# Kernel tuning notes

Measured on AMD Instinct MI355X. Metric: run time of the kernel, lower is better.

The kernel has to match this reference:

```python
import jax, jax.numpy as jnp
import numpy as np

D = 512          # model_dim
H = 4 * D        # hidden_mult * model_dim
E = 8            # n_experts
TEMP = 1.0       # temperature
EPS = 1e-5       # torch LayerNorm eps


def setup_inputs() -> dict:
    key = jax.random.key(0)
    ks = jax.random.split(key, 6)
    x = jax.random.normal(ks[0], (4, 4096, D), dtype=jnp.float32)
    # gate: LayerNorm(D) + Linear(D, E)
    gate_gamma = jnp.ones((D,), jnp.float32)
    gate_beta = jnp.zeros((D,), jnp.float32)
    gate_W = jax.random.normal(ks[1], (D, E), jnp.float32) * 0.02
    gate_b = jnp.zeros((E,), jnp.float32)
    # experts stacked along leading E axis: Linear(D,H) -> LeakyReLU -> Linear(H,D)
    W1 = jax.random.normal(ks[2], (E, D, H), jnp.float32) * 0.02
    b1 = jnp.zeros((E, H), jnp.float32)
    W2 = jax.random.normal(ks[3], (E, H, D), jnp.float32) * 0.02
    b2 = jnp.zeros((E, D), jnp.float32)
    return {"x": x, "gate_gamma": gate_gamma, "gate_beta": gate_beta,
            "gate_W": gate_W, "gate_b": gate_b,
            "W1": W1, "b1": b1, "W2": W2, "b2": b2}


def reference(x, gate_gamma, gate_beta, gate_W, gate_b, W1, b1, W2, b2):
    # gate: LayerNorm then Linear, temperature-scaled softmax
    mu = jnp.mean(x, axis=-1, keepdims=True)
    var = jnp.var(x, axis=-1, keepdims=True)  # biased, as in torch LayerNorm
    xn = (x - mu) * jax.lax.rsqrt(var + EPS) * gate_gamma + gate_beta
    logits = (xn @ gate_W + gate_b) / TEMP          # [B,N,E]
    w = jax.nn.softmax(logits, axis=-1)             # [B,N,E]
    # run every expert on all tokens (faithful to soft routing)
    h = jnp.einsum('bnd,edh->benh', x, W1) + b1[None, :, None, :]  # [B,E,N,H]
    h = jax.nn.leaky_relu(h, negative_slope=0.01)
    y = jnp.einsum('benh,ehd->bend', h, W2) + b2[None, :, None, :]  # [B,E,N,D]
    # gate-weighted combine over experts
    out = jnp.einsum('bend,bne->bnd', y, w)
    return out
```

## Files before the change

kernel.cpp:

```cpp
#include <hip/hip_runtime.h>
#include <stdint.h>

#define TD 512
#define TH 2048
#define TE 8
#define TT 16384

typedef __bf16 bf16x8 __attribute__((ext_vector_type(8)));
typedef float  f32x4  __attribute__((ext_vector_type(4)));

__device__ __forceinline__ void async16(const void* src, void* lds) {
    __builtin_amdgcn_global_load_lds((const __attribute__((address_space(1))) uint32_t*)src,
                                     (__attribute__((address_space(3))) uint32_t*)lds,
                                     16, 0, 0);
}

__global__ __launch_bounds__(256) void gate_kernel(
    const float* __restrict__ x, const float* __restrict__ gamma,
    const float* __restrict__ beta, const float* __restrict__ gW,
    const float* __restrict__ gb, const float* __restrict__ b2,
    float* __restrict__ gate_w, __bf16* __restrict__ xb,
    float* __restrict__ outp)
{
    const int t    = blockIdx.x * 4 + (threadIdx.x >> 6);
    const int lane = threadIdx.x & 63;

    const float* xr = x + (size_t)t * TD + lane * 8;
    float4 v0 = *(const float4*)xr;
    float4 v1 = *(const float4*)(xr + 4);
    float xv[8] = {v0.x, v0.y, v0.z, v0.w, v1.x, v1.y, v1.z, v1.w};

    float s = 0.f, sq = 0.f;
    #pragma unroll
    for (int j = 0; j < 8; ++j) { s += xv[j]; sq += xv[j] * xv[j]; }
    #pragma unroll
    for (int off = 32; off > 0; off >>= 1) {
        s  += __shfl_xor(s, off);
        sq += __shfl_xor(sq, off);
    }
    const float mean = s * (1.f / TD);
    const float var  = sq * (1.f / TD) - mean * mean;
    const float rs   = rsqrtf(var + 1e-5f);

    bf16x8 xc;
    #pragma unroll
    for (int j = 0; j < 8; ++j) xc[j] = (__bf16)xv[j];
    *(bf16x8*)&xb[(size_t)t * TD + lane * 8] = xc;

    float p[TE] = {};
    #pragma unroll
    for (int j = 0; j < 8; ++j) {
        const int d = lane * 8 + j;
        const float xn = (xv[j] - mean) * rs * gamma[d] + beta[d];
        const float* wr = gW + (size_t)d * TE;
        #pragma unroll
        for (int e = 0; e < TE; ++e) p[e] += xn * wr[e];
    }
    #pragma unroll
    for (int off = 32; off > 0; off >>= 1) {
        #pragma unroll
        for (int e = 0; e < TE; ++e) p[e] += __shfl_xor(p[e], off);
    }

    float m = -3.4e38f;
    #pragma unroll
    for (int e = 0; e < TE; ++e) { p[e] += gb[e]; m = fmaxf(m, p[e]); }
    float sum = 0.f;
    #pragma unroll
    for (int e = 0; e < TE; ++e) { p[e] = expf(p[e] - m); sum += p[e]; }
    const float inv = 1.f / sum;
    if (lane == 0) {
        #pragma unroll
        for (int e = 0; e < TE; ++e) gate_w[(size_t)t * TE + e] = p[e] * inv;
    }

    float ob[8] = {};
    #pragma unroll
    for (int e = 0; e < TE; ++e) {
        const float we = p[e] * inv;
        const float* b2r = b2 + (size_t)e * TD + lane * 8;
        #pragma unroll
        for (int j = 0; j < 8; ++j) ob[j] += we * b2r[j];
    }
    float4 o0 = {ob[0], ob[1], ob[2], ob[3]};
    float4 o1 = {ob[4], ob[5], ob[6], ob[7]};
    *(float4*)&outp[(size_t)t * TD + lane * 8]     = o0;
    *(float4*)&outp[(size_t)t * TD + lane * 8 + 4] = o1;
}

__global__ __launch_bounds__(256) void tcast(
    const float* __restrict__ src, __bf16* __restrict__ dst, int R, int C)
{
    __shared__ __bf16 tile[64][65];
    const int e  = blockIdx.z;
    const int r0 = blockIdx.y * 64, c0 = blockIdx.x * 64;
    const int tr = threadIdx.x >> 6;
    const int tc = threadIdx.x & 63;

    const float* s = src + ((size_t)e * R + r0) * C + c0;
    #pragma unroll
    for (int i = 0; i < 16; ++i) {
        const int r = i * 4 + tr;
        tile[r][tc] = (__bf16)s[(size_t)r * C + tc];
    }
    __syncthreads();
    __bf16* d = dst + ((size_t)e * C + c0) * R + r0;
    #pragma unroll
    for (int i = 0; i < 16; ++i) {
        const int c = i * 4 + tr;
        d[(size_t)c * R + tc] = tile[tc][c];
    }
}

template <int EPI>
__global__ __launch_bounds__(512, 2) void gemm8p(
    const __bf16* __restrict__ A, const __bf16* __restrict__ Bt,
    const float* __restrict__ bias, const float* __restrict__ gw,
    void* __restrict__ C, int K, int e)
{
    __shared__ __align__(16) char smem[131072];
    const int tid  = threadIdx.x;
    const int w    = tid >> 6, lane = tid & 63;
    const int wr   = w >> 2, wc = w & 3;
    const int fr   = lane & 15, ks = lane >> 4;

    int bm, bn;
    if (EPI == 0) {
        bn = blockIdx.x & 7;
        bm = blockIdx.x >> 3;
    } else {
        const int xcd = blockIdx.x & 7, idx = blockIdx.x >> 3;
        bn = xcd >> 2;
        const int sub  = xcd & 3;
        const int eloc = idx >> 4;
        bm = sub * 16 + (idx & 15);
        A  += (size_t)eloc * TT * TH;
        Bt += (size_t)eloc * TD * TH;
        e = eloc;
    }

    const __bf16* Ab = A  + (size_t)bm * 256 * K;
    const __bf16* Bb = Bt + (size_t)bn * 256 * K;
    const int NT = K >> 6;

    f32x4 acc[8][4] = {};

    auto stage = [&](int h) {
        const int th = h >> 2, j = h & 3;
        const int mat = j & 1, hks = j >> 1, hbuf = th & 1;
        const __bf16* mb = mat ? Bb : Ab;
        char* region = smem + mat * 65536 + hbuf * 32768 + hks * 16384;
        #pragma unroll
        for (int i = 0; i < 2; ++i) {
            const int cid = i * 512 + tid;
            const int row = cid >> 2;
            const int gc  = (cid & 3) ^ ((row >> 1) & 3);
            async16(mb + (size_t)row * K + th * 64 + hks * 32 + gc * 8,
                    region + i * 8192 + w * 1024);
        }
    };

    #pragma unroll
    for (int h = 0; h < 6; ++h) stage(h);
    asm volatile("s_waitcnt vmcnt(8)" ::: "memory");
    __builtin_amdgcn_sched_barrier(0);
    __builtin_amdgcn_s_barrier();

    bf16x8 areg[8];

    for (int t = 0; t < NT; ++t) {
        const int buf = t & 1;
        const char* aB = smem + buf * 32768;
        const char* bB = smem + 65536 + buf * 32768;
        #pragma unroll
        for (int q = 0; q < 4; ++q) {
            const int kst = q >> 1, nh = q & 1;
            const char* aR = aB + kst * 16384;
            const char* bR = bB + kst * 16384;
            if (nh == 0) {
                #pragma unroll
                for (int m = 0; m < 8; ++m) {
                    const int row = wr * 128 + m * 16 + fr;
                    areg[m] = *(const bf16x8*)(aR + row * 64 + (((ks ^ (row >> 1)) & 3) << 4));
                }
            }
            bf16x8 bf0, bf1;
            {
                const int r0 = wc * 64 + nh * 32 + fr;
                const int r1 = r0 + 16;
                bf0 = *(const bf16x8*)(bR + r0 * 64 + (((ks ^ (r0 >> 1)) & 3) << 4));
                bf1 = *(const bf16x8*)(bR + r1 * 64 + (((ks ^ (r1 >> 1)) & 3) << 4));
            }
            const int h = t * 4 + q + 6;
            if (h < NT * 4) stage(h);
            if (nh == 1) { asm volatile("s_waitcnt vmcnt(8)" ::: "memory"); }
            __builtin_amdgcn_sched_barrier(0);
            __builtin_amdgcn_s_barrier();
            asm volatile("s_waitcnt lgkmcnt(0)" ::: "memory");
            __builtin_amdgcn_sched_barrier(0);
            __builtin_amdgcn_s_setprio(1);
            #pragma unroll
            for (int m = 0; m < 8; ++m) {
                acc[m][nh*2+0] = __builtin_amdgcn_mfma_f32_16x16x32_bf16(areg[m], bf0, acc[m][nh*2+0], 0, 0, 0);
                acc[m][nh*2+1] = __builtin_amdgcn_mfma_f32_16x16x32_bf16(areg[m], bf1, acc[m][nh*2+1], 0, 0, 0);
            }
            __builtin_amdgcn_s_setprio(0);
            __builtin_amdgcn_sched_barrier(0);
            __builtin_amdgcn_s_barrier();
        }
    }

    const int rj = (lane >> 4) << 2;
    if (EPI == 0) {
        __bf16* hC = (__bf16*)C;
        #pragma unroll
        for (int m = 0; m < 8; ++m) {
            const int gr0 = bm * 256 + wr * 128 + m * 16 + rj;
            #pragma unroll
            for (int j = 0; j < 4; ++j) {
                const int gr = gr0 + j;
                const float wgt = gw[(size_t)gr * TE + e];
                #pragma unroll
                for (int n = 0; n < 4; ++n) {
                    const int gc = bn * 256 + wc * 64 + n * 16 + fr;
                    float v = acc[m][n][j] + bias[gc];
                    v = v > 0.f ? v : 0.01f * v;
                    hC[(size_t)gr * TH + gc] = (__bf16)(v * wgt);
                }
            }
        }
    } else {
        float* oC = (float*)C;
        #pragma unroll
        for (int m = 0; m < 8; ++m) {
            const int gr0 = bm * 256 + wr * 128 + m * 16 + rj;
            #pragma unroll
            for (int j = 0; j < 4; ++j) {
                const int gr = gr0 + j;
                #pragma unroll
                for (int n = 0; n < 4; ++n) {
                    const int gc = bn * 256 + wc * 64 + n * 16 + fr;
                    atomicAdd(oC + (size_t)gr * TD + gc, acc[m][n][j]);
                }
            }
        }
    }
}

extern "C" void kernel_launch(void* const* d_in, const int* in_sizes, int n_in,
                              void* d_out, int out_size, void* d_ws, size_t ws_size,
                              hipStream_t stream)
{
    const float* x     = (const float*)d_in[0];
    const float* gamma = (const float*)d_in[1];
    const float* beta  = (const float*)d_in[2];
    const float* gW    = (const float*)d_in[3];
    const float* gb    = (const float*)d_in[4];
    const float* W1    = (const float*)d_in[5];
    const float* b1    = (const float*)d_in[6];
    const float* W2    = (const float*)d_in[7];
    const float* b2    = (const float*)d_in[8];

    char* ws = (char*)d_ws;
    size_t off = 0;
    float*  gate_w = (float*)(ws + off);  off += (size_t)TT * TE * 4;
    __bf16* xb     = (__bf16*)(ws + off); off += (size_t)TT * TD * 2;
    __bf16* W1t    = (__bf16*)(ws + off); off += (size_t)TE * TD * TH * 2;
    __bf16* W2t    = (__bf16*)(ws + off); off += (size_t)TE * TD * TH * 2;
    __bf16* hg     = (__bf16*)(ws + off);

    gate_kernel<<<TT / 4, 256, 0, stream>>>(x, gamma, beta, gW, gb, b2,
                                            gate_w, xb, (float*)d_out);
    tcast<<<dim3(TH / 64, TD / 64, TE), 256, 0, stream>>>(W1, W1t, TD, TH);
    tcast<<<dim3(TD / 64, TH / 64, TE), 256, 0, stream>>>(W2, W2t, TH, TD);

    for (int g = 0; g < 4; ++g) {
        #pragma unroll
        for (int s = 0; s < 2; ++s) {
            const int e = 2 * g + s;
            gemm8p<0><<<512, 512, 0, stream>>>(
                xb, W1t + (size_t)e * TH * TD, b1 + (size_t)e * TH, gate_w,
                (void*)(hg + (size_t)s * TT * TH), TD , e);
        }
        gemm8p<1><<<256, 512, 0, stream>>>(
            hg, W2t + (size_t)(2 * g) * TD * TH, nullptr, nullptr,
            d_out, TH , 0);
    }
}
```

Before: 883.1 us.

## Merge expert pairs into single GEMM launches with concatenated K layout

Each pair of experts now runs as one 1024-block first GEMM instead of two launches. Hidden activations are written in a [T, 2*H] interleaved layout, and W2 is transposed into a matching concatenated-K layout, so the second GEMM reads both experts as one contiguous 4096-wide reduction split into K halves. The first GEMM swaps its MFMA operands so that each lane holds four consecutive columns, which lets the epilogue load the bias as a vector and write packed bf16x4 values. Block-to-XCD mapping is also reworked, and K and stride become compile-time constants.

```diff
diff --git a/kernel.cpp b/kernel.cpp
--- a/kernel.cpp
+++ b/kernel.cpp
@@ -7,6 +7,7 @@
 #define TT 16384
 
 typedef __bf16 bf16x8 __attribute__((ext_vector_type(8)));
+typedef __bf16 bf16x4 __attribute__((ext_vector_type(4)));
 typedef float  f32x4  __attribute__((ext_vector_type(4)));
 
 __device__ __forceinline__ void async16(const void* src, void* lds) {
@@ -88,6 +89,7 @@
     *(float4*)&outp[(size_t)t * TD + lane * 8 + 4] = o1;
 }
 
+template <int MODE>
 __global__ __launch_bounds__(256) void tcast(
     const float* __restrict__ src, __bf16* __restrict__ dst, int R, int C)
 {
@@ -104,44 +106,56 @@
         tile[r][tc] = (__bf16)s[(size_t)r * C + tc];
     }
     __syncthreads();
-    __bf16* d = dst + ((size_t)e * C + c0) * R + r0;
+
+    size_t RS, eoff;
+    if (MODE == 0) { RS = (size_t)R;     eoff = (size_t)e * C * R; }
+    else           { RS = (size_t)2 * R; eoff = (size_t)(e >> 1) * C * 2 * R + (size_t)(e & 1) * R; }
+
+    __bf16* d = dst + eoff + (size_t)c0 * RS + r0;
     #pragma unroll
     for (int i = 0; i < 16; ++i) {
         const int c = i * 4 + tr;
-        d[(size_t)c * R + tc] = tile[tc][c];
+        d[(size_t)c * RS + tc] = tile[tc][c];
     }
 }
 
 template <int EPI>
 __global__ __launch_bounds__(512, 2) void gemm8p(
     const __bf16* __restrict__ A, const __bf16* __restrict__ Bt,
-    const float* __restrict__ bias, const float* __restrict__ gw,
-    void* __restrict__ C, int K, int e)
+    const float* __restrict__ b1, const float* __restrict__ gw,
+    void* __restrict__ C, int grp)
 {
+    constexpr int K = (EPI == 0) ? TD : TH;
+    constexpr int S = (EPI == 0) ? TD : 2 * TH;
+    constexpr int NT = K >> 6;
+
     __shared__ __align__(16) char smem[131072];
     const int tid  = threadIdx.x;
     const int w    = tid >> 6, lane = tid & 63;
     const int wr   = w >> 2, wc = w & 3;
     const int fr   = lane & 15, ks = lane >> 4;
 
-    int bm, bn;
+    int bm, bn, e2 = 0, e = 0;
     if (EPI == 0) {
-        bn = blockIdx.x & 7;
-        bm = blockIdx.x >> 3;
+        const int xcd = blockIdx.x & 7, idx = blockIdx.x >> 3;
+        bm = xcd * 8 + (idx & 7);
+        e2 = (idx >> 3) & 1;
+        bn = idx >> 4;
+        e  = grp * 2 + e2;
+        A  += (size_t)bm * 256 * S;
+        Bt += (size_t)e2 * TH * TD + (size_t)bn * 256 * S;
+        b1 += (size_t)e * TH;
     } else {
         const int xcd = blockIdx.x & 7, idx = blockIdx.x >> 3;
-        bn = xcd >> 2;
-        const int sub  = xcd & 3;
-        const int eloc = idx >> 4;
-        bm = sub * 16 + (idx & 15);
-        A  += (size_t)eloc * TT * TH;
-        Bt += (size_t)eloc * TD * TH;
-        e = eloc;
-    }
-
-    const __bf16* Ab = A  + (size_t)bm * 256 * K;
-    const __bf16* Bb = Bt + (size_t)bn * 256 * K;
-    const int NT = K >> 6;
+        bn = xcd & 1;
+        bm = (xcd >> 1) * 16 + (idx & 15);
+        const int kh = idx >> 4;
+        A  += (size_t)bm * 256 * S + (size_t)kh * 2048;
+        Bt += (size_t)bn * 256 * S + (size_t)kh * 2048;
+    }
+
+    const __bf16* Ab = A;
+    const __bf16* Bb = Bt;
 
     f32x4 acc[8][4] = {};
 
@@ -155,7 +169,7 @@
             const int cid = i * 512 + tid;
             const int row = cid >> 2;
             const int gc  = (cid & 3) ^ ((row >> 1) & 3);
-            async16(mb + (size_t)row * K + th * 64 + hks * 32 + gc * 8,
+            async16(mb + (size_t)row * S + th * 64 + hks * 32 + gc * 8,
                     region + i * 8192 + w * 1024);
         }
     };
@@ -201,8 +215,13 @@
             __builtin_amdgcn_s_setprio(1);
             #pragma unroll
             for (int m = 0; m < 8; ++m) {
-                acc[m][nh*2+0] = __builtin_amdgcn_mfma_f32_16x16x32_bf16(areg[m], bf0, acc[m][nh*2+0], 0, 0, 0);
-                acc[m][nh*2+1] = __builtin_amdgcn_mfma_f32_16x16x32_bf16(areg[m], bf1, acc[m][nh*2+1], 0, 0, 0);
+                if (EPI == 0) {
+                    acc[m][nh*2+0] = __builtin_amdgcn_mfma_f32_16x16x32_bf16(bf0, areg[m], acc[m][nh*2+0], 0, 0, 0);
+                    acc[m][nh*2+1] = __builtin_amdgcn_mfma_f32_16x16x32_bf16(bf1, areg[m], acc[m][nh*2+1], 0, 0, 0);
+                } else {
+                    acc[m][nh*2+0] = __builtin_amdgcn_mfma_f32_16x16x32_bf16(areg[m], bf0, acc[m][nh*2+0], 0, 0, 0);
+                    acc[m][nh*2+1] = __builtin_amdgcn_mfma_f32_16x16x32_bf16(areg[m], bf1, acc[m][nh*2+1], 0, 0, 0);
+                }
             }
             __builtin_amdgcn_s_setprio(0);
             __builtin_amdgcn_sched_barrier(0);
@@ -210,27 +229,31 @@
         }
     }
 
-    const int rj = (lane >> 4) << 2;
     if (EPI == 0) {
         __bf16* hC = (__bf16*)C;
+        const int rjc = (lane >> 4) << 2;
         #pragma unroll
         for (int m = 0; m < 8; ++m) {
-            const int gr0 = bm * 256 + wr * 128 + m * 16 + rj;
+            const int row = bm * 256 + wr * 128 + m * 16 + fr;
+            const float wgt = gw[(size_t)row * TE + e];
+            __bf16* hrow = hC + (size_t)row * (2 * TH) + e2 * TH;
             #pragma unroll
-            for (int j = 0; j < 4; ++j) {
-                const int gr = gr0 + j;
-                const float wgt = gw[(size_t)gr * TE + e];
+            for (int n = 0; n < 4; ++n) {
+                const int colb = bn * 256 + wc * 64 + n * 16 + rjc;
+                const f32x4 bv = *(const f32x4*)&b1[colb];
+                bf16x4 ov;
                 #pragma unroll
-                for (int n = 0; n < 4; ++n) {
-                    const int gc = bn * 256 + wc * 64 + n * 16 + fr;
-                    float v = acc[m][n][j] + bias[gc];
+                for (int j = 0; j < 4; ++j) {
+                    float v = acc[m][n][j] + bv[j];
                     v = v > 0.f ? v : 0.01f * v;
-                    hC[(size_t)gr * TH + gc] = (__bf16)(v * wgt);
+                    ov[j] = (__bf16)(v * wgt);
                 }
+                *(bf16x4*)&hrow[colb] = ov;
             }
         }
     } else {
         float* oC = (float*)C;
+        const int rj = (lane >> 4) << 2;
         #pragma unroll
         for (int m = 0; m < 8; ++m) {
             const int gr0 = bm * 256 + wr * 128 + m * 16 + rj;
@@ -266,24 +289,18 @@
     float*  gate_w = (float*)(ws + off);  off += (size_t)TT * TE * 4;
     __bf16* xb     = (__bf16*)(ws + off); off += (size_t)TT * TD * 2;
     __bf16* W1t    = (__bf16*)(ws + off); off += (size_t)TE * TD * TH * 2;
-    __bf16* W2t    = (__bf16*)(ws + off); off += (size_t)TE * TD * TH * 2;
-    __bf16* hg     = (__bf16*)(ws + off);
+    __bf16* W2tc   = (__bf16*)(ws + off); off += (size_t)TE * TD * TH * 2;
+    __bf16* h      = (__bf16*)(ws + off);
 
     gate_kernel<<<TT / 4, 256, 0, stream>>>(x, gamma, beta, gW, gb, b2,
                                             gate_w, xb, (float*)d_out);
-    tcast<<<dim3(TH / 64, TD / 64, TE), 256, 0, stream>>>(W1, W1t, TD, TH);
-    tcast<<<dim3(TD / 64, TH / 64, TE), 256, 0, stream>>>(W2, W2t, TH, TD);
-
-    for (int g = 0; g < 4; ++g) {
-        #pragma unroll
-        for (int s = 0; s < 2; ++s) {
-            const int e = 2 * g + s;
-            gemm8p<0><<<512, 512, 0, stream>>>(
-                xb, W1t + (size_t)e * TH * TD, b1 + (size_t)e * TH, gate_w,
-                (void*)(hg + (size_t)s * TT * TH), TD , e);
-        }
+    tcast<0><<<dim3(TH / 64, TD / 64, TE), 256, 0, stream>>>(W1, W1t, TD, TH);
+    tcast<1><<<dim3(TD / 64, TH / 64, TE), 256, 0, stream>>>(W2, W2tc, TH, TD);
+
+    for (int grp = 0; grp < 4; ++grp) {
+        gemm8p<0><<<1024, 512, 0, stream>>>(
+            xb, W1t + (size_t)grp * 2 * TH * TD, b1, gate_w, (void*)h, grp);
         gemm8p<1><<<256, 512, 0, stream>>>(
-            hg, W2t + (size_t)(2 * g) * TD * TH, nullptr, nullptr,
-            d_out, TH , 0);
-    }
-}
+            h, W2tc + (size_t)grp * TD * 2 * TH, nullptr, nullptr, d_out, grp);
+    }
+}
```

After: 858.4 us. 1.03x faster.
